# Performance work log

Hardware: AMD Instinct MI355X
Metric: run time of the kernel (lower is better)

Reference implementation:

```python
import jax, jax.numpy as jnp
import numpy as np

N_PARTS = 4
HIDDEN = 256
NUM_FREQS = 10
IN_DIM = 3
EMB_DIM = IN_DIM * (1 + 2 * NUM_FREQS)  # 63
PART_DIM = HIDDEN // N_PARTS


def _embed(x):
    freqs = 2.0 ** jnp.arange(NUM_FREQS, dtype=x.dtype)        # [F]
    xf = x[..., None, :] * freqs[:, None]                      # [..., F, 3]
    enc = jnp.stack([jnp.sin(xf), jnp.cos(xf)], axis=-2)       # [..., F, 2, 3]
    enc = enc.reshape(x.shape[:-1] + (NUM_FREQS * 2 * IN_DIM,))
    return jnp.concatenate([x, enc], axis=-1)                  # [..., 63]


def _masks():
    # contiguous 0/1 per-part neuron masks over the HIDDEN axis (ClassMaskCreator)
    m = np.zeros((N_PARTS, HIDDEN), dtype=np.float32)
    for p in range(N_PARTS):
        s = p * PART_DIM
        e = HIDDEN if p == N_PARTS - 1 else s + PART_DIM
        m[p, s:e] = 1.0
    return jnp.asarray(m)


def setup_inputs() -> dict:
    key = jax.random.key(0)
    ks = jax.random.split(key, 8)
    B, N = 1, 131072

    def lin(k, fan_in, fan_out):
        return jax.random.normal(k, (fan_in, fan_out), jnp.float32) / np.float32(np.sqrt(fan_in))

    return {
        "coords": jax.random.normal(ks[0], (B, N, IN_DIM), jnp.float32),
        "W0": lin(ks[1], EMB_DIM, HIDDEN), "b0": jnp.zeros((HIDDEN,), jnp.float32),
        "W1": lin(ks[2], HIDDEN, HIDDEN), "b1": jnp.zeros((HIDDEN,), jnp.float32),
        "W2": lin(ks[3], HIDDEN, HIDDEN), "b2": jnp.zeros((HIDDEN,), jnp.float32),
        "Wocc": lin(ks[4], HIDDEN, 1), "bocc": jnp.zeros((1,), jnp.float32),
        "Wc": jax.random.normal(ks[5], (N_PARTS, HIDDEN), jnp.float32) / np.float32(np.sqrt(HIDDEN)),
        "bc": jnp.zeros((N_PARTS,), jnp.float32),
    }


def reference(coords, W0, b0, W1, b1, W2, b2, Wocc, bocc, Wc, bc):
    masks = _masks()                                  # [P, H]
    x = _embed(coords) @ W0 + b0                      # [B, N, H]  (no activation after layer 0, per source)

    # occupancy trunk: relu(L1) -> relu(L2) -> occ head
    x_occ = jax.nn.relu(x @ W1 + b1)
    x_occ = jax.nn.relu(x_occ @ W2 + b2)
    occ = x_occ @ Wocc + bocc                         # [B, N, 1]

    # part branches. Loop iteration i=0 masks x; i=1 indexes temporal_part_output[1*part_id],
    # i.e. the i=0 outputs. The i=1 outputs (h2) are dead w.r.t. all returned values because
    # part_features[part_id] for part_id in 0..P-1 selects the first P (i=0) entries.
    h1 = [jax.nn.relu((x * masks[p]) @ W1 + b1) for p in range(N_PARTS)]  # [B, N, H] each

    # class heads: class_heads[p](h1[p] * mask_p).squeeze(0), concatenated on last dim
    cls = [jnp.squeeze((h1[p] * masks[p]) @ Wc[p][:, None] + bc[p], axis=0)
           for p in range(N_PARTS)]                   # [N, 1] each (B == 1)
    part_class = jnp.concatenate(cls, axis=-1)        # [N, P]

    return occ, part_class
```

## Files before the change

kernel.cpp:

```cpp
#include <hip/hip_runtime.h>


#define NPTS 131072
#define M_PB 128
#define AST 256

typedef _Float16 half8   __attribute__((ext_vector_type(8)));
typedef _Float16 half4_t __attribute__((ext_vector_type(4)));
typedef __fp16   fp16x2  __attribute__((ext_vector_type(2)));
typedef float    float4_t __attribute__((ext_vector_type(4)));

__global__ void prep(const float* __restrict__ W0, const float* __restrict__ W1,
                     const float* __restrict__ W2, _Float16* __restrict__ ws) {
  int id = blockIdx.x * 256 + threadIdx.x;
  _Float16 v;
  if (id < 16384) {
    int e = id, j = e & 7, l = (e >> 3) & 63, tn = (e >> 9) & 3, kb = (e >> 11) & 1, s = e >> 12;
    int k = kb * 32 + (l >> 4) * 8 + j, n = s * 64 + tn * 16 + (l & 15);
    v = (k < 63) ? (_Float16)W0[k * 256 + n] : (_Float16)0.f;
  } else if (id < 81920) {
    int e = id - 16384, j = e & 7, l = (e >> 3) & 63, tn = (e >> 9) & 3, kb = (e >> 11) & 7, s = e >> 14;
    int k = kb * 32 + (l >> 4) * 8 + j, n = s * 64 + tn * 16 + (l & 15);
    v = (_Float16)W1[k * 256 + n];
  } else {
    int e = id - 81920, j = e & 7, l = (e >> 3) & 63, tn = (e >> 9) & 3, kb = (e >> 11) & 7, s = e >> 14;
    int k = kb * 32 + (l >> 4) * 8 + j, n = s * 64 + tn * 16 + (l & 15);
    v = (_Float16)W2[k * 256 + n];
  }
  ws[id] = v;
}

__device__ __forceinline__ half4_t pack4(float a, float b, float cc, float d) {
  fp16x2 p0 = __builtin_amdgcn_cvt_pkrtz(a, b);
  fp16x2 p1 = __builtin_amdgcn_cvt_pkrtz(cc, d);
  half4_t h;
  h[0] = (_Float16)p0[0]; h[1] = (_Float16)p0[1];
  h[2] = (_Float16)p1[0]; h[3] = (_Float16)p1[1];
  return h;
}

__global__ __launch_bounds__(256, 2) void mlp_main(
    const float* __restrict__ coords,
    const _Float16* __restrict__ W0sw,
    const _Float16* __restrict__ W1sw,
    const _Float16* __restrict__ W2sw,
    const float* __restrict__ b0, const float* __restrict__ b1,
    const float* __restrict__ b2,
    const float* __restrict__ Wocc, const float* __restrict__ bocc,
    const float* __restrict__ Wc, const float* __restrict__ bc,
    float* __restrict__ out) {
  __shared__ _Float16 actX[M_PB * AST];
  __shared__ float occ_s[4][M_PB];

  const int t = threadIdx.x;
  const int w = t >> 6;
  const int l = t & 63;
  const int c = l & 15;
  const int q = l >> 4;
  const int sx = c & 7;
  const int m0 = blockIdx.x * M_PB;

  half8 a0[4], a1[4];
  {
    const _Float16* wb = W0sw + (size_t)w * 4096 + l * 8;
#pragma unroll
    for (int tn = 0; tn < 4; ++tn) {
      a0[tn] = *(const half8*)(wb + tn * 512);
      a1[tn] = *(const half8*)(wb + 2048 + tn * 512);
    }
  }

  {
    int m = t & 127, kh = (t >> 7) * 32;
    const int cb = (t >> 7) * 4;
    const int sm = m & 7;
    const float* cp = coords + (size_t)(m0 + m) * 3;
    float x0 = cp[0], x1 = cp[1], x2 = cp[2];
#pragma unroll
    for (int i = 0; i < 4; ++i) {
      float v[8];
#pragma unroll
      for (int u = 0; u < 8; ++u) {
        int k = kh + i * 8 + u;
        float r;
        if (k >= 63) r = 0.f;
        else if (k < 3) r = (k == 0) ? x0 : (k == 1 ? x1 : x2);
        else {
          int kk = k - 3;
          int f = kk / 6;
          int rem = kk - 6 * f;
          int s = (rem >= 3) ? 1 : 0;
          int i3 = rem - 3 * s;
          float xi = (i3 == 0) ? x0 : (i3 == 1 ? x1 : x2);
          float arg = xi * (float)(1 << f);
          float nn = rintf(arg * 0.15915494309189535f);
          float rr = fmaf(nn, -6.28318548202514648f, arg);
          rr = fmaf(nn, 1.7484555e-7f, rr);
          r = s ? __cosf(rr) : __sinf(rr);
        }
        v[u] = r;
      }
      half8 ev;
#pragma unroll
      for (int u = 0; u < 4; ++u) {
        fp16x2 p = __builtin_amdgcn_cvt_pkrtz(v[2 * u], v[2 * u + 1]);
        ev[2 * u] = (_Float16)p[0]; ev[2 * u + 1] = (_Float16)p[1];
      }
      *(half8*)&actX[m * AST + (((cb + i) ^ sm) << 3)] = ev;
    }
  }
  __syncthreads();

  float4_t acc[4][8];
  const _Float16* rp = actX + c * AST;

  {
#pragma unroll
    for (int tn = 0; tn < 4; ++tn) {
      float4_t bz = *(const float4_t*)(b0 + 64 * w + tn * 16 + q * 4);
#pragma unroll
      for (int tm = 0; tm < 8; ++tm) acc[tn][tm] = bz;
    }
#pragma unroll
    for (int kb = 0; kb < 2; ++kb) {
      const int cx = ((kb * 4 + q) ^ sx) << 3;
      half8 b[8];
#pragma unroll
      for (int tm = 0; tm < 8; ++tm) b[tm] = *(const half8*)(rp + tm * 16 * AST + cx);
#pragma unroll
      for (int tn = 0; tn < 4; ++tn)
#pragma unroll
        for (int tm = 0; tm < 8; ++tm)
          acc[tn][tm] = __builtin_amdgcn_mfma_f32_16x16x32_f16(
              kb ? a1[tn] : a0[tn], b[tm], acc[tn][tm], 0, 0, 0);
    }
  }
  __syncthreads();
#pragma unroll
  for (int tn = 0; tn < 4; ++tn) {
    const int sc = ((8 * w + 2 * tn + (q >> 1)) ^ sx) * 8 + (q & 1) * 4;
#pragma unroll
    for (int tm = 0; tm < 8; ++tm) {
      float4_t v = acc[tn][tm];
      *(half4_t*)&actX[(tm * 16 + c) * AST + sc] = pack4(v[0], v[1], v[2], v[3]);
    }
  }
  __syncthreads();

  {
    const _Float16* wb = W1sw + (size_t)w * 16384 + l * 8;
    const int w2 = 2 * w;
    float bcw = bc[w];
#pragma unroll
    for (int tn = 0; tn < 4; ++tn) {
      float4_t bz = *(const float4_t*)(b1 + 64 * w + tn * 16 + q * 4);
#pragma unroll
      for (int tm = 0; tm < 8; ++tm) acc[tn][tm] = bz;
    }
    auto kbof = [&](int j) {
      return (j < 2) ? (w2 + j) : ((j - 2) + ((j - 2) >= w2 ? 2 : 0));
    };
    half8 A[3][4];
#pragma unroll
    for (int p = 0; p < 3; ++p) {
      const _Float16* pa = wb + kbof(p) * 2048;
#pragma unroll
      for (int tn = 0; tn < 4; ++tn) A[p][tn] = *(const half8*)(pa + tn * 512);
    }
#pragma unroll
    for (int j = 0; j < 8; ++j) {
      const int kb = kbof(j);
      const int cx = ((kb * 4 + q) ^ sx) << 3;
      half8 b[8];
#pragma unroll
      for (int tm = 0; tm < 8; ++tm) b[tm] = *(const half8*)(rp + tm * 16 * AST + cx);
#pragma unroll
      for (int tn = 0; tn < 4; ++tn)
#pragma unroll
        for (int tm = 0; tm < 8; ++tm)
          acc[tn][tm] = __builtin_amdgcn_mfma_f32_16x16x32_f16(
              A[j % 3][tn], b[tm], acc[tn][tm], 0, 0, 0);
      if (j == 1) {
        float pcls[8] = {0.f, 0.f, 0.f, 0.f, 0.f, 0.f, 0.f, 0.f};
#pragma unroll
        for (int tn = 0; tn < 4; ++tn) {
          float4_t wcv = *(const float4_t*)(Wc + 256 * w + 64 * w + tn * 16 + q * 4);
#pragma unroll
          for (int tm = 0; tm < 8; ++tm) {
            float4_t v = acc[tn][tm];
#pragma unroll
            for (int r = 0; r < 4; ++r) pcls[tm] += fmaxf(v[r], 0.f) * wcv[r];
          }
        }
#pragma unroll
        for (int tm = 0; tm < 8; ++tm) {
          float s = pcls[tm];
          s += __shfl_xor(s, 16, 64);
          s += __shfl_xor(s, 32, 64);
          if (l < 16)
            out[(size_t)NPTS + (size_t)(m0 + tm * 16 + c) * 4 + w] = s + bcw;
        }
      }
      if (j + 3 < 8) {
        const _Float16* pa = wb + kbof(j + 3) * 2048;
#pragma unroll
        for (int tn = 0; tn < 4; ++tn) A[j % 3][tn] = *(const half8*)(pa + tn * 512);
      }
    }
  }
  __syncthreads();
#pragma unroll
  for (int tn = 0; tn < 4; ++tn) {
    const int sc = ((8 * w + 2 * tn + (q >> 1)) ^ sx) * 8 + (q & 1) * 4;
#pragma unroll
    for (int tm = 0; tm < 8; ++tm) {
      float4_t v = acc[tn][tm];
      *(half4_t*)&actX[(tm * 16 + c) * AST + sc] =
          pack4(fmaxf(v[0], 0.f), fmaxf(v[1], 0.f), fmaxf(v[2], 0.f), fmaxf(v[3], 0.f));
    }
  }
  __syncthreads();

  {
    const _Float16* wb = W2sw + (size_t)w * 16384 + l * 8;
#pragma unroll
    for (int tn = 0; tn < 4; ++tn) {
      float4_t bz = *(const float4_t*)(b2 + 64 * w + tn * 16 + q * 4);
#pragma unroll
      for (int tm = 0; tm < 8; ++tm) acc[tn][tm] = bz;
    }
    half8 A[3][4];
#pragma unroll
    for (int p = 0; p < 3; ++p)
#pragma unroll
      for (int tn = 0; tn < 4; ++tn)
        A[p][tn] = *(const half8*)(wb + p * 2048 + tn * 512);
#pragma unroll
    for (int kb = 0; kb < 8; ++kb) {
      const int cx = ((kb * 4 + q) ^ sx) << 3;
      half8 b[8];
#pragma unroll
      for (int tm = 0; tm < 8; ++tm) b[tm] = *(const half8*)(rp + tm * 16 * AST + cx);
#pragma unroll
      for (int tn = 0; tn < 4; ++tn)
#pragma unroll
        for (int tm = 0; tm < 8; ++tm)
          acc[tn][tm] = __builtin_amdgcn_mfma_f32_16x16x32_f16(
              A[kb % 3][tn], b[tm], acc[tn][tm], 0, 0, 0);
      if (kb + 3 < 8) {
#pragma unroll
        for (int tn = 0; tn < 4; ++tn)
          A[kb % 3][tn] = *(const half8*)(wb + (kb + 3) * 2048 + tn * 512);
      }
    }
    float pocc[8] = {0.f, 0.f, 0.f, 0.f, 0.f, 0.f, 0.f, 0.f};
#pragma unroll
    for (int tn = 0; tn < 4; ++tn) {
      float4_t wov = *(const float4_t*)(Wocc + 64 * w + tn * 16 + q * 4);
#pragma unroll
      for (int tm = 0; tm < 8; ++tm) {
        float4_t v = acc[tn][tm];
#pragma unroll
        for (int r = 0; r < 4; ++r) pocc[tm] += fmaxf(v[r], 0.f) * wov[r];
      }
    }
#pragma unroll
    for (int tm = 0; tm < 8; ++tm) {
      float s = pocc[tm];
      s += __shfl_xor(s, 16, 64);
      s += __shfl_xor(s, 32, 64);
      if (l < 16) occ_s[w][tm * 16 + c] = s;
    }
  }
  __syncthreads();
  if (t < M_PB) {
    out[m0 + t] = occ_s[0][t] + occ_s[1][t] + occ_s[2][t] + occ_s[3][t] + bocc[0];
  }
}

extern "C" void kernel_launch(void* const* d_in, const int* in_sizes, int n_in,
                              void* d_out, int out_size, void* d_ws, size_t ws_size,
                              hipStream_t stream) {
  const float* coords = (const float*)d_in[0];
  const float* W0   = (const float*)d_in[1];
  const float* b0   = (const float*)d_in[2];
  const float* W1   = (const float*)d_in[3];
  const float* b1   = (const float*)d_in[4];
  const float* W2   = (const float*)d_in[5];
  const float* b2   = (const float*)d_in[6];
  const float* Wocc = (const float*)d_in[7];
  const float* bocc = (const float*)d_in[8];
  const float* Wc   = (const float*)d_in[9];
  const float* bc   = (const float*)d_in[10];
  float* out = (float*)d_out;

  _Float16* ws = (_Float16*)d_ws;
  _Float16* W0sw = ws;
  _Float16* W1sw = ws + 16384;
  _Float16* W2sw = ws + 81920;

  prep<<<576, 256, 0, stream>>>(W0, W1, W2, ws);
  mlp_main<<<NPTS / M_PB, 256, 0, stream>>>(coords, W0sw, W1sw, W2sw,
                                            b0, b1, b2, Wocc, bocc, Wc, bc, out);
}
```

Baseline: 116.9 us.

## Ping-pong two warp groups across staggered MLP phases in 512-thread blocks

The kernel now launches 512-thread blocks, each holding two 256-thread groups with separate shared-memory activation buffers. Each block processes four 128-point tiles in a staggered schedule: one group runs the embedding and layer-0 phase while the other runs the layer-1 and layer-2 MFMA phases. The aim is to overlap the transcendental and VALU work with matrix-core work, and s_setprio is raised around the MFMA loops. In exchange, shared memory per block doubles, block-wide barriers now couple the two groups, and idle stagger steps are added at the start and end of the schedule.

```diff
diff --git a/kernel.cpp b/kernel.cpp
--- a/kernel.cpp
+++ b/kernel.cpp
@@ -39,7 +39,7 @@
   return h;
 }
 
-__global__ __launch_bounds__(256, 2) void mlp_main(
+__global__ __launch_bounds__(512, 2) void mlp_main(
     const float* __restrict__ coords,
     const _Float16* __restrict__ W0sw,
     const _Float16* __restrict__ W1sw,
@@ -49,232 +49,251 @@
     const float* __restrict__ Wocc, const float* __restrict__ bocc,
     const float* __restrict__ Wc, const float* __restrict__ bc,
     float* __restrict__ out) {
-  __shared__ _Float16 actX[M_PB * AST];
-  __shared__ float occ_s[4][M_PB];
+  __shared__ _Float16 actX[2][M_PB * AST];
+  __shared__ float occ_s[2][4][M_PB];
 
   const int t = threadIdx.x;
-  const int w = t >> 6;
+  const int g = t >> 8;
+  const int tl = t & 255;
+  const int w = (t >> 6) & 3;
   const int l = t & 63;
   const int c = l & 15;
   const int q = l >> 4;
   const int sx = c & 7;
-  const int m0 = blockIdx.x * M_PB;
-
+  const int blockBase = blockIdx.x * 512;
+
+  _Float16* aX = actX[g];
+  const _Float16* rp = aX + c * AST;
+
+  float4_t acc[4][8];
   half8 a0[4], a1[4];
-  {
-    const _Float16* wb = W0sw + (size_t)w * 4096 + l * 8;
-#pragma unroll
-    for (int tn = 0; tn < 4; ++tn) {
-      a0[tn] = *(const half8*)(wb + tn * 512);
-      a1[tn] = *(const half8*)(wb + 2048 + tn * 512);
+
+#pragma unroll 1
+  for (int i = 0; i < 5; ++i) {
+    const int step = i - g;
+    const bool isAct = (step >= 0) && (step < 4);
+    const bool isA = isAct && ((step & 1) == 0);
+    const bool isB = isAct && ((step & 1) == 1);
+    const int sp = isAct ? step : 0;
+    const int m0 = blockBase + 128 * (g + 2 * (sp >> 1));
+
+    if (isA) {
+      {
+        const _Float16* wb = W0sw + (size_t)w * 4096 + l * 8;
+#pragma unroll
+        for (int tn = 0; tn < 4; ++tn) {
+          a0[tn] = *(const half8*)(wb + tn * 512);
+          a1[tn] = *(const half8*)(wb + 2048 + tn * 512);
+        }
+      }
+      int m = tl & 127, kh = (tl >> 7) * 32;
+      const int cb = (tl >> 7) * 4;
+      const int sm = m & 7;
+      const float* cp = coords + (size_t)(m0 + m) * 3;
+      float x0 = cp[0], x1 = cp[1], x2 = cp[2];
+#pragma unroll
+      for (int ii = 0; ii < 4; ++ii) {
+        float v[8];
+#pragma unroll
+        for (int u = 0; u < 8; ++u) {
+          int k = kh + ii * 8 + u;
+          float r;
+          if (k >= 63) r = 0.f;
+          else if (k < 3) r = (k == 0) ? x0 : (k == 1 ? x1 : x2);
+          else {
+            int kk = k - 3;
+            int f = kk / 6;
+            int rem = kk - 6 * f;
+            int s = (rem >= 3) ? 1 : 0;
+            int i3 = rem - 3 * s;
+            float xi = (i3 == 0) ? x0 : (i3 == 1 ? x1 : x2);
+            float arg = xi * (float)(1 << f);
+            float nn = rintf(arg * 0.15915494309189535f);
+            float rr = fmaf(nn, -6.28318548202514648f, arg);
+            rr = fmaf(nn, 1.7484555e-7f, rr);
+            r = s ? __cosf(rr) : __sinf(rr);
+          }
+          v[u] = r;
+        }
+        half8 ev;
+#pragma unroll
+        for (int u = 0; u < 4; ++u) {
+          fp16x2 p = __builtin_amdgcn_cvt_pkrtz(v[2 * u], v[2 * u + 1]);
+          ev[2 * u] = (_Float16)p[0]; ev[2 * u + 1] = (_Float16)p[1];
+        }
+        *(half8*)&aX[m * AST + (((cb + ii) ^ sm) << 3)] = ev;
+      }
+    } else if (isB) {
+      const _Float16* wb = W1sw + (size_t)w * 16384 + l * 8;
+      const int w2 = 2 * w;
+      float bcw = bc[w];
+#pragma unroll
+      for (int tn = 0; tn < 4; ++tn) {
+        float4_t bz = *(const float4_t*)(b1 + 64 * w + tn * 16 + q * 4);
+#pragma unroll
+        for (int tm = 0; tm < 8; ++tm) acc[tn][tm] = bz;
+      }
+      auto kbof = [&](int j) {
+        return (j < 2) ? (w2 + j) : ((j - 2) + ((j - 2) >= w2 ? 2 : 0));
+      };
+      half8 A[3][4];
+#pragma unroll
+      for (int p = 0; p < 3; ++p) {
+        const _Float16* pa = wb + kbof(p) * 2048;
+#pragma unroll
+        for (int tn = 0; tn < 4; ++tn) A[p][tn] = *(const half8*)(pa + tn * 512);
+      }
+#pragma unroll
+      for (int j = 0; j < 8; ++j) {
+        const int kb = kbof(j);
+        const int cx = ((kb * 4 + q) ^ sx) << 3;
+        half8 b[8];
+#pragma unroll
+        for (int tm = 0; tm < 8; ++tm) b[tm] = *(const half8*)(rp + tm * 16 * AST + cx);
+        __builtin_amdgcn_s_setprio(1);
+#pragma unroll
+        for (int tn = 0; tn < 4; ++tn)
+#pragma unroll
+          for (int tm = 0; tm < 8; ++tm)
+            acc[tn][tm] = __builtin_amdgcn_mfma_f32_16x16x32_f16(
+                A[j % 3][tn], b[tm], acc[tn][tm], 0, 0, 0);
+        __builtin_amdgcn_s_setprio(0);
+        if (j == 1) {
+          float pcls[8] = {0.f, 0.f, 0.f, 0.f, 0.f, 0.f, 0.f, 0.f};
+#pragma unroll
+          for (int tn = 0; tn < 4; ++tn) {
+            float4_t wcv = *(const float4_t*)(Wc + 256 * w + 64 * w + tn * 16 + q * 4);
+#pragma unroll
+            for (int tm = 0; tm < 8; ++tm) {
+              float4_t v = acc[tn][tm];
+#pragma unroll
+              for (int r = 0; r < 4; ++r) pcls[tm] += fmaxf(v[r], 0.f) * wcv[r];
+            }
+          }
+#pragma unroll
+          for (int tm = 0; tm < 8; ++tm) {
+            float s = pcls[tm];
+            s += __shfl_xor(s, 16, 64);
+            s += __shfl_xor(s, 32, 64);
+            if (l < 16)
+              out[(size_t)NPTS + (size_t)(m0 + tm * 16 + c) * 4 + w] = s + bcw;
+          }
+        }
+        if (j + 3 < 8) {
+          const _Float16* pa = wb + kbof(j + 3) * 2048;
+#pragma unroll
+          for (int tn = 0; tn < 4; ++tn) A[j % 3][tn] = *(const half8*)(pa + tn * 512);
+        }
+      }
     }
-  }
-
-  {
-    int m = t & 127, kh = (t >> 7) * 32;
-    const int cb = (t >> 7) * 4;
-    const int sm = m & 7;
-    const float* cp = coords + (size_t)(m0 + m) * 3;
-    float x0 = cp[0], x1 = cp[1], x2 = cp[2];
-#pragma unroll
-    for (int i = 0; i < 4; ++i) {
-      float v[8];
-#pragma unroll
-      for (int u = 0; u < 8; ++u) {
-        int k = kh + i * 8 + u;
-        float r;
-        if (k >= 63) r = 0.f;
-        else if (k < 3) r = (k == 0) ? x0 : (k == 1 ? x1 : x2);
-        else {
-          int kk = k - 3;
-          int f = kk / 6;
-          int rem = kk - 6 * f;
-          int s = (rem >= 3) ? 1 : 0;
-          int i3 = rem - 3 * s;
-          float xi = (i3 == 0) ? x0 : (i3 == 1 ? x1 : x2);
-          float arg = xi * (float)(1 << f);
-          float nn = rintf(arg * 0.15915494309189535f);
-          float rr = fmaf(nn, -6.28318548202514648f, arg);
-          rr = fmaf(nn, 1.7484555e-7f, rr);
-          r = s ? __cosf(rr) : __sinf(rr);
-        }
-        v[u] = r;
-      }
-      half8 ev;
-#pragma unroll
-      for (int u = 0; u < 4; ++u) {
-        fp16x2 p = __builtin_amdgcn_cvt_pkrtz(v[2 * u], v[2 * u + 1]);
-        ev[2 * u] = (_Float16)p[0]; ev[2 * u + 1] = (_Float16)p[1];
-      }
-      *(half8*)&actX[m * AST + (((cb + i) ^ sm) << 3)] = ev;
+    __syncthreads();
+
+    if (isA) {
+#pragma unroll
+      for (int tn = 0; tn < 4; ++tn) {
+        float4_t bz = *(const float4_t*)(b0 + 64 * w + tn * 16 + q * 4);
+#pragma unroll
+        for (int tm = 0; tm < 8; ++tm) acc[tn][tm] = bz;
+      }
+#pragma unroll
+      for (int kb = 0; kb < 2; ++kb) {
+        const int cx = ((kb * 4 + q) ^ sx) << 3;
+        half8 b[8];
+#pragma unroll
+        for (int tm = 0; tm < 8; ++tm) b[tm] = *(const half8*)(rp + tm * 16 * AST + cx);
+#pragma unroll
+        for (int tn = 0; tn < 4; ++tn)
+#pragma unroll
+          for (int tm = 0; tm < 8; ++tm)
+            acc[tn][tm] = __builtin_amdgcn_mfma_f32_16x16x32_f16(
+                kb ? a1[tn] : a0[tn], b[tm], acc[tn][tm], 0, 0, 0);
+      }
+    } else if (isB) {
+#pragma unroll
+      for (int tn = 0; tn < 4; ++tn) {
+        const int sc = ((8 * w + 2 * tn + (q >> 1)) ^ sx) * 8 + (q & 1) * 4;
+#pragma unroll
+        for (int tm = 0; tm < 8; ++tm) {
+          float4_t v = acc[tn][tm];
+          *(half4_t*)&aX[(tm * 16 + c) * AST + sc] =
+              pack4(fmaxf(v[0], 0.f), fmaxf(v[1], 0.f), fmaxf(v[2], 0.f), fmaxf(v[3], 0.f));
+        }
+      }
     }
-  }
-  __syncthreads();
-
-  float4_t acc[4][8];
-  const _Float16* rp = actX + c * AST;
-
-  {
-#pragma unroll
-    for (int tn = 0; tn < 4; ++tn) {
-      float4_t bz = *(const float4_t*)(b0 + 64 * w + tn * 16 + q * 4);
-#pragma unroll
-      for (int tm = 0; tm < 8; ++tm) acc[tn][tm] = bz;
+    __syncthreads();
+
+    if (isA) {
+#pragma unroll
+      for (int tn = 0; tn < 4; ++tn) {
+        const int sc = ((8 * w + 2 * tn + (q >> 1)) ^ sx) * 8 + (q & 1) * 4;
+#pragma unroll
+        for (int tm = 0; tm < 8; ++tm) {
+          float4_t v = acc[tn][tm];
+          *(half4_t*)&aX[(tm * 16 + c) * AST + sc] = pack4(v[0], v[1], v[2], v[3]);
+        }
+      }
+    } else if (isB) {
+      const _Float16* wb = W2sw + (size_t)w * 16384 + l * 8;
+#pragma unroll
+      for (int tn = 0; tn < 4; ++tn) {
+        float4_t bz = *(const float4_t*)(b2 + 64 * w + tn * 16 + q * 4);
+#pragma unroll
+        for (int tm = 0; tm < 8; ++tm) acc[tn][tm] = bz;
+      }
+      half8 A[3][4];
+#pragma unroll
+      for (int p = 0; p < 3; ++p)
+#pragma unroll
+        for (int tn = 0; tn < 4; ++tn)
+          A[p][tn] = *(const half8*)(wb + p * 2048 + tn * 512);
+#pragma unroll
+      for (int kb = 0; kb < 8; ++kb) {
+        const int cx = ((kb * 4 + q) ^ sx) << 3;
+        half8 b[8];
+#pragma unroll
+        for (int tm = 0; tm < 8; ++tm) b[tm] = *(const half8*)(rp + tm * 16 * AST + cx);
+        __builtin_amdgcn_s_setprio(1);
+#pragma unroll
+        for (int tn = 0; tn < 4; ++tn)
+#pragma unroll
+          for (int tm = 0; tm < 8; ++tm)
+            acc[tn][tm] = __builtin_amdgcn_mfma_f32_16x16x32_f16(
+                A[kb % 3][tn], b[tm], acc[tn][tm], 0, 0, 0);
+        __builtin_amdgcn_s_setprio(0);
+        if (kb + 3 < 8) {
+#pragma unroll
+          for (int tn = 0; tn < 4; ++tn)
+            A[kb % 3][tn] = *(const half8*)(wb + (kb + 3) * 2048 + tn * 512);
+        }
+      }
+      float pocc[8] = {0.f, 0.f, 0.f, 0.f, 0.f, 0.f, 0.f, 0.f};
+#pragma unroll
+      for (int tn = 0; tn < 4; ++tn) {
+        float4_t wov = *(const float4_t*)(Wocc + 64 * w + tn * 16 + q * 4);
+#pragma unroll
+        for (int tm = 0; tm < 8; ++tm) {
+          float4_t v = acc[tn][tm];
+#pragma unroll
+          for (int r = 0; r < 4; ++r) pocc[tm] += fmaxf(v[r], 0.f) * wov[r];
+        }
+      }
+#pragma unroll
+      for (int tm = 0; tm < 8; ++tm) {
+        float s = pocc[tm];
+        s += __shfl_xor(s, 16, 64);
+        s += __shfl_xor(s, 32, 64);
+        if (l < 16) occ_s[g][w][tm * 16 + c] = s;
+      }
     }
-#pragma unroll
-    for (int kb = 0; kb < 2; ++kb) {
-      const int cx = ((kb * 4 + q) ^ sx) << 3;
-      half8 b[8];
-#pragma unroll
-      for (int tm = 0; tm < 8; ++tm) b[tm] = *(const half8*)(rp + tm * 16 * AST + cx);
-#pragma unroll
-      for (int tn = 0; tn < 4; ++tn)
-#pragma unroll
-        for (int tm = 0; tm < 8; ++tm)
-          acc[tn][tm] = __builtin_amdgcn_mfma_f32_16x16x32_f16(
-              kb ? a1[tn] : a0[tn], b[tm], acc[tn][tm], 0, 0, 0);
+    __syncthreads();
+
+    if (isB) {
+      if (tl < M_PB) {
+        out[m0 + tl] = occ_s[g][0][tl] + occ_s[g][1][tl] +
+                       occ_s[g][2][tl] + occ_s[g][3][tl] + bocc[0];
+      }
     }
-  }
-  __syncthreads();
-#pragma unroll
-  for (int tn = 0; tn < 4; ++tn) {
-    const int sc = ((8 * w + 2 * tn + (q >> 1)) ^ sx) * 8 + (q & 1) * 4;
-#pragma unroll
-    for (int tm = 0; tm < 8; ++tm) {
-      float4_t v = acc[tn][tm];
-      *(half4_t*)&actX[(tm * 16 + c) * AST + sc] = pack4(v[0], v[1], v[2], v[3]);
-    }
-  }
-  __syncthreads();
-
-  {
-    const _Float16* wb = W1sw + (size_t)w * 16384 + l * 8;
-    const int w2 = 2 * w;
-    float bcw = bc[w];
-#pragma unroll
-    for (int tn = 0; tn < 4; ++tn) {
-      float4_t bz = *(const float4_t*)(b1 + 64 * w + tn * 16 + q * 4);
-#pragma unroll
-      for (int tm = 0; tm < 8; ++tm) acc[tn][tm] = bz;
-    }
-    auto kbof = [&](int j) {
-      return (j < 2) ? (w2 + j) : ((j - 2) + ((j - 2) >= w2 ? 2 : 0));
-    };
-    half8 A[3][4];
-#pragma unroll
-    for (int p = 0; p < 3; ++p) {
-      const _Float16* pa = wb + kbof(p) * 2048;
-#pragma unroll
-      for (int tn = 0; tn < 4; ++tn) A[p][tn] = *(const half8*)(pa + tn * 512);
-    }
-#pragma unroll
-    for (int j = 0; j < 8; ++j) {
-      const int kb = kbof(j);
-      const int cx = ((kb * 4 + q) ^ sx) << 3;
-      half8 b[8];
-#pragma unroll
-      for (int tm = 0; tm < 8; ++tm) b[tm] = *(const half8*)(rp + tm * 16 * AST + cx);
-#pragma unroll
-      for (int tn = 0; tn < 4; ++tn)
-#pragma unroll
-        for (int tm = 0; tm < 8; ++tm)
-          acc[tn][tm] = __builtin_amdgcn_mfma_f32_16x16x32_f16(
-              A[j % 3][tn], b[tm], acc[tn][tm], 0, 0, 0);
-      if (j == 1) {
-        float pcls[8] = {0.f, 0.f, 0.f, 0.f, 0.f, 0.f, 0.f, 0.f};
-#pragma unroll
-        for (int tn = 0; tn < 4; ++tn) {
-          float4_t wcv = *(const float4_t*)(Wc + 256 * w + 64 * w + tn * 16 + q * 4);
-#pragma unroll
-          for (int tm = 0; tm < 8; ++tm) {
-            float4_t v = acc[tn][tm];
-#pragma unroll
-            for (int r = 0; r < 4; ++r) pcls[tm] += fmaxf(v[r], 0.f) * wcv[r];
-          }
-        }
-#pragma unroll
-        for (int tm = 0; tm < 8; ++tm) {
-          float s = pcls[tm];
-          s += __shfl_xor(s, 16, 64);
-          s += __shfl_xor(s, 32, 64);
-          if (l < 16)
-            out[(size_t)NPTS + (size_t)(m0 + tm * 16 + c) * 4 + w] = s + bcw;
-        }
-      }
-      if (j + 3 < 8) {
-        const _Float16* pa = wb + kbof(j + 3) * 2048;
-#pragma unroll
-        for (int tn = 0; tn < 4; ++tn) A[j % 3][tn] = *(const half8*)(pa + tn * 512);
-      }
-    }
-  }
-  __syncthreads();
-#pragma unroll
-  for (int tn = 0; tn < 4; ++tn) {
-    const int sc = ((8 * w + 2 * tn + (q >> 1)) ^ sx) * 8 + (q & 1) * 4;
-#pragma unroll
-    for (int tm = 0; tm < 8; ++tm) {
-      float4_t v = acc[tn][tm];
-      *(half4_t*)&actX[(tm * 16 + c) * AST + sc] =
-          pack4(fmaxf(v[0], 0.f), fmaxf(v[1], 0.f), fmaxf(v[2], 0.f), fmaxf(v[3], 0.f));
-    }
-  }
-  __syncthreads();
-
-  {
-    const _Float16* wb = W2sw + (size_t)w * 16384 + l * 8;
-#pragma unroll
-    for (int tn = 0; tn < 4; ++tn) {
-      float4_t bz = *(const float4_t*)(b2 + 64 * w + tn * 16 + q * 4);
-#pragma unroll
-      for (int tm = 0; tm < 8; ++tm) acc[tn][tm] = bz;
-    }
-    half8 A[3][4];
-#pragma unroll
-    for (int p = 0; p < 3; ++p)
-#pragma unroll
-      for (int tn = 0; tn < 4; ++tn)
-        A[p][tn] = *(const half8*)(wb + p * 2048 + tn * 512);
-#pragma unroll
-    for (int kb = 0; kb < 8; ++kb) {
-      const int cx = ((kb * 4 + q) ^ sx) << 3;
-      half8 b[8];
-#pragma unroll
-      for (int tm = 0; tm < 8; ++tm) b[tm] = *(const half8*)(rp + tm * 16 * AST + cx);
-#pragma unroll
-      for (int tn = 0; tn < 4; ++tn)
-#pragma unroll
-        for (int tm = 0; tm < 8; ++tm)
-          acc[tn][tm] = __builtin_amdgcn_mfma_f32_16x16x32_f16(
-              A[kb % 3][tn], b[tm], acc[tn][tm], 0, 0, 0);
-      if (kb + 3 < 8) {
-#pragma unroll
-        for (int tn = 0; tn < 4; ++tn)
-          A[kb % 3][tn] = *(const half8*)(wb + (kb + 3) * 2048 + tn * 512);
-      }
-    }
-    float pocc[8] = {0.f, 0.f, 0.f, 0.f, 0.f, 0.f, 0.f, 0.f};
-#pragma unroll
-    for (int tn = 0; tn < 4; ++tn) {
-      float4_t wov = *(const float4_t*)(Wocc + 64 * w + tn * 16 + q * 4);
-#pragma unroll
-      for (int tm = 0; tm < 8; ++tm) {
-        float4_t v = acc[tn][tm];
-#pragma unroll
-        for (int r = 0; r < 4; ++r) pocc[tm] += fmaxf(v[r], 0.f) * wov[r];
-      }
-    }
-#pragma unroll
-    for (int tm = 0; tm < 8; ++tm) {
-      float s = pocc[tm];
-      s += __shfl_xor(s, 16, 64);
-      s += __shfl_xor(s, 32, 64);
-      if (l < 16) occ_s[w][tm * 16 + c] = s;
-    }
-  }
-  __syncthreads();
-  if (t < M_PB) {
-    out[m0 + t] = occ_s[0][t] + occ_s[1][t] + occ_s[2][t] + occ_s[3][t] + bocc[0];
+    __syncthreads();
   }
 }
 
@@ -300,6 +319,6 @@
   _Float16* W2sw = ws + 81920;
 
   prep<<<576, 256, 0, stream>>>(W0, W1, W2, ws);
-  mlp_main<<<NPTS / M_PB, 256, 0, stream>>>(coords, W0sw, W1sw, W2sw,
-                                            b0, b1, b2, Wocc, bocc, Wc, bc, out);
+  mlp_main<<<NPTS / 512, 512, 0, stream>>>(coords, W0sw, W1sw, W2sw,
+                                           b0, b1, b2, Wocc, bocc, Wc, bc, out);
 }
```

Measured after the change: 221.1 us. 89.1% more time.

## Split positional encoding into a separate kernel and load MFMA operands directly

Applied to the files above, without the earlier changes.

Adds a standalone kernel that computes the fp16 positional encoding for all points into workspace. The main MLP kernel then loads the layer-0 B operands straight from global memory into registers, which removes the in-kernel sin/cos work and the LDS staging and sync before layer 0. The intent is to shorten the serial prologue of each block. The cost is an extra launch and a global round trip of about 16 MB of encoding, and the old path is kept as a fallback when the workspace is too small.

```diff
diff --git a/kernel.cpp b/kernel.cpp
--- a/kernel.cpp
+++ b/kernel.cpp
@@ -31,15 +31,260 @@
 }
 
 __device__ __forceinline__ half4_t pack4(float a, float b, float cc, float d) {
-  fp16x2 p0 = __builtin_amdgcn_cvt_pkrtz(a, b);
-  fp16x2 p1 = __builtin_amdgcn_cvt_pkrtz(cc, d);
-  half4_t h;
-  h[0] = (_Float16)p0[0]; h[1] = (_Float16)p0[1];
-  h[2] = (_Float16)p1[0]; h[3] = (_Float16)p1[1];
-  return h;
-}
-
-__global__ __launch_bounds__(256, 2) void mlp_main(
+  union { half4_t h; fp16x2 p[2]; } u;
+  u.p[0] = __builtin_amdgcn_cvt_pkrtz(a, b);
+  u.p[1] = __builtin_amdgcn_cvt_pkrtz(cc, d);
+  return u.h;
+}
+
+__device__ __forceinline__ float pe_val(int k, float x0, float x1, float x2) {
+  float r;
+  if (k >= 63) r = 0.f;
+  else if (k < 3) r = (k == 0) ? x0 : (k == 1 ? x1 : x2);
+  else {
+    int kk = k - 3;
+    int f = kk / 6;
+    int rem = kk - 6 * f;
+    int s = (rem >= 3) ? 1 : 0;
+    int i3 = rem - 3 * s;
+    float xi = (i3 == 0) ? x0 : (i3 == 1 ? x1 : x2);
+    float arg = xi * (float)(1 << f);
+    float nn = rintf(arg * 0.15915494309189535f);
+    float rr = fmaf(nn, -6.28318548202514648f, arg);
+    rr = fmaf(nn, 1.7484555e-7f, rr);
+    r = s ? __cosf(rr) : __sinf(rr);
+  }
+  return r;
+}
+
+__global__ __launch_bounds__(256) void pe(const float* __restrict__ coords,
+                                          _Float16* __restrict__ eg) {
+  int id = blockIdx.x * 256 + threadIdx.x;
+  int m = id >> 2, s = id & 3;
+  const float* cp = coords + (size_t)m * 3;
+  float x0 = cp[0], x1 = cp[1], x2 = cp[2];
+  int kh = s * 16;
+#pragma unroll
+  for (int i = 0; i < 2; ++i) {
+    float v[8];
+#pragma unroll
+    for (int u = 0; u < 8; ++u) v[u] = pe_val(kh + i * 8 + u, x0, x1, x2);
+    half8 ev;
+#pragma unroll
+    for (int u = 0; u < 4; ++u) {
+      fp16x2 p = __builtin_amdgcn_cvt_pkrtz(v[2 * u], v[2 * u + 1]);
+      ev[2 * u] = (_Float16)p[0]; ev[2 * u + 1] = (_Float16)p[1];
+    }
+    *(half8*)(eg + (size_t)m * 64 + kh + i * 8) = ev;
+  }
+}
+
+__global__ __launch_bounds__(256, 2) void mlp_main_g(
+    const _Float16* __restrict__ eg,
+    const _Float16* __restrict__ W0sw,
+    const _Float16* __restrict__ W1sw,
+    const _Float16* __restrict__ W2sw,
+    const float* __restrict__ b0, const float* __restrict__ b1,
+    const float* __restrict__ b2,
+    const float* __restrict__ Wocc, const float* __restrict__ bocc,
+    const float* __restrict__ Wc, const float* __restrict__ bc,
+    float* __restrict__ out) {
+  __shared__ _Float16 actX[M_PB * AST];
+  __shared__ float occ_s[4][M_PB];
+
+  const int t = threadIdx.x;
+  const int w = t >> 6;
+  const int l = t & 63;
+  const int c = l & 15;
+  const int q = l >> 4;
+  const int sx = c & 7;
+  const int m0 = blockIdx.x * M_PB;
+
+  half8 e0[8], e1[8];
+  {
+    const _Float16* ep = eg + (size_t)(m0 + c) * 64 + q * 8;
+#pragma unroll
+    for (int tm = 0; tm < 8; ++tm) {
+      e0[tm] = *(const half8*)(ep + tm * 1024);
+      e1[tm] = *(const half8*)(ep + tm * 1024 + 32);
+    }
+  }
+  half8 a0[4], a1[4];
+  {
+    const _Float16* wb = W0sw + (size_t)w * 4096 + l * 8;
+#pragma unroll
+    for (int tn = 0; tn < 4; ++tn) {
+      a0[tn] = *(const half8*)(wb + tn * 512);
+      a1[tn] = *(const half8*)(wb + 2048 + tn * 512);
+    }
+  }
+
+  float4_t acc[4][8];
+  const _Float16* rp = actX + c * AST;
+
+  {
+#pragma unroll
+    for (int tn = 0; tn < 4; ++tn) {
+      float4_t bz = *(const float4_t*)(b0 + 64 * w + tn * 16 + q * 4);
+#pragma unroll
+      for (int tm = 0; tm < 8; ++tm) acc[tn][tm] = bz;
+    }
+#pragma unroll
+    for (int tn = 0; tn < 4; ++tn)
+#pragma unroll
+      for (int tm = 0; tm < 8; ++tm)
+        acc[tn][tm] = __builtin_amdgcn_mfma_f32_16x16x32_f16(
+            a0[tn], e0[tm], acc[tn][tm], 0, 0, 0);
+#pragma unroll
+    for (int tn = 0; tn < 4; ++tn)
+#pragma unroll
+      for (int tm = 0; tm < 8; ++tm)
+        acc[tn][tm] = __builtin_amdgcn_mfma_f32_16x16x32_f16(
+            a1[tn], e1[tm], acc[tn][tm], 0, 0, 0);
+  }
+#pragma unroll
+  for (int tn = 0; tn < 4; ++tn) {
+    const int sc = ((8 * w + 2 * tn + (q >> 1)) ^ sx) * 8 + (q & 1) * 4;
+#pragma unroll
+    for (int tm = 0; tm < 8; ++tm) {
+      float4_t v = acc[tn][tm];
+      *(half4_t*)&actX[(tm * 16 + c) * AST + sc] = pack4(v[0], v[1], v[2], v[3]);
+    }
+  }
+  __syncthreads();
+
+  {
+    const _Float16* wb = W1sw + (size_t)w * 16384 + l * 8;
+    const int w2 = 2 * w;
+    float bcw = bc[w];
+#pragma unroll
+    for (int tn = 0; tn < 4; ++tn) {
+      float4_t bz = *(const float4_t*)(b1 + 64 * w + tn * 16 + q * 4);
+#pragma unroll
+      for (int tm = 0; tm < 8; ++tm) acc[tn][tm] = bz;
+    }
+    auto kbof = [&](int j) {
+      return (j < 2) ? (w2 + j) : ((j - 2) + ((j - 2) >= w2 ? 2 : 0));
+    };
+    half8 A[3][4];
+#pragma unroll
+    for (int p = 0; p < 3; ++p) {
+      const _Float16* pa = wb + kbof(p) * 2048;
+#pragma unroll
+      for (int tn = 0; tn < 4; ++tn) A[p][tn] = *(const half8*)(pa + tn * 512);
+    }
+#pragma unroll
+    for (int j = 0; j < 8; ++j) {
+      const int kb = kbof(j);
+      const int cx = ((kb * 4 + q) ^ sx) << 3;
+      half8 b[8];
+#pragma unroll
+      for (int tm = 0; tm < 8; ++tm) b[tm] = *(const half8*)(rp + tm * 16 * AST + cx);
+#pragma unroll
+      for (int tn = 0; tn < 4; ++tn)
+#pragma unroll
+        for (int tm = 0; tm < 8; ++tm)
+          acc[tn][tm] = __builtin_amdgcn_mfma_f32_16x16x32_f16(
+              A[j % 3][tn], b[tm], acc[tn][tm], 0, 0, 0);
+      if (j == 1) {
+        float pcls[8] = {0.f, 0.f, 0.f, 0.f, 0.f, 0.f, 0.f, 0.f};
+#pragma unroll
+        for (int tn = 0; tn < 4; ++tn) {
+          float4_t wcv = *(const float4_t*)(Wc + 256 * w + 64 * w + tn * 16 + q * 4);
+#pragma unroll
+          for (int tm = 0; tm < 8; ++tm) {
+            float4_t v = acc[tn][tm];
+#pragma unroll
+            for (int r = 0; r < 4; ++r) pcls[tm] += fmaxf(v[r], 0.f) * wcv[r];
+          }
+        }
+#pragma unroll
+        for (int tm = 0; tm < 8; ++tm) {
+          float s = pcls[tm];
+          s += __shfl_xor(s, 16, 64);
+          s += __shfl_xor(s, 32, 64);
+          if (l < 16)
+            out[(size_t)NPTS + (size_t)(m0 + tm * 16 + c) * 4 + w] = s + bcw;
+        }
+      }
+      if (j + 3 < 8) {
+        const _Float16* pa = wb + kbof(j + 3) * 2048;
+#pragma unroll
+        for (int tn = 0; tn < 4; ++tn) A[j % 3][tn] = *(const half8*)(pa + tn * 512);
+      }
+    }
+  }
+  __syncthreads();
+#pragma unroll
+  for (int tn = 0; tn < 4; ++tn) {
+    const int sc = ((8 * w + 2 * tn + (q >> 1)) ^ sx) * 8 + (q & 1) * 4;
+#pragma unroll
+    for (int tm = 0; tm < 8; ++tm) {
+      float4_t v = acc[tn][tm];
+      *(half4_t*)&actX[(tm * 16 + c) * AST + sc] =
+          pack4(fmaxf(v[0], 0.f), fmaxf(v[1], 0.f), fmaxf(v[2], 0.f), fmaxf(v[3], 0.f));
+    }
+  }
+  __syncthreads();
+
+  {
+    const _Float16* wb = W2sw + (size_t)w * 16384 + l * 8;
+#pragma unroll
+    for (int tn = 0; tn < 4; ++tn) {
+      float4_t bz = *(const float4_t*)(b2 + 64 * w + tn * 16 + q * 4);
+#pragma unroll
+      for (int tm = 0; tm < 8; ++tm) acc[tn][tm] = bz;
+    }
+    half8 A[3][4];
+#pragma unroll
+    for (int p = 0; p < 3; ++p)
+#pragma unroll
+      for (int tn = 0; tn < 4; ++tn)
+        A[p][tn] = *(const half8*)(wb + p * 2048 + tn * 512);
+#pragma unroll
+    for (int kb = 0; kb < 8; ++kb) {
+      const int cx = ((kb * 4 + q) ^ sx) << 3;
+      half8 b[8];
+#pragma unroll
+      for (int tm = 0; tm < 8; ++tm) b[tm] = *(const half8*)(rp + tm * 16 * AST + cx);
+#pragma unroll
+      for (int tn = 0; tn < 4; ++tn)
+#pragma unroll
+        for (int tm = 0; tm < 8; ++tm)
+          acc[tn][tm] = __builtin_amdgcn_mfma_f32_16x16x32_f16(
+              A[kb % 3][tn], b[tm], acc[tn][tm], 0, 0, 0);
+      if (kb + 3 < 8) {
+#pragma unroll
+        for (int tn = 0; tn < 4; ++tn)
+          A[kb % 3][tn] = *(const half8*)(wb + (kb + 3) * 2048 + tn * 512);
+      }
+    }
+    float pocc[8] = {0.f, 0.f, 0.f, 0.f, 0.f, 0.f, 0.f, 0.f};
+#pragma unroll
+    for (int tn = 0; tn < 4; ++tn) {
+      float4_t wov = *(const float4_t*)(Wocc + 64 * w + tn * 16 + q * 4);
+#pragma unroll
+      for (int tm = 0; tm < 8; ++tm) {
+        float4_t v = acc[tn][tm];
+#pragma unroll
+        for (int r = 0; r < 4; ++r) pocc[tm] += fmaxf(v[r], 0.f) * wov[r];
+      }
+    }
+#pragma unroll
+    for (int tm = 0; tm < 8; ++tm) {
+      float s = pocc[tm];
+      s += __shfl_xor(s, 16, 64);
+      s += __shfl_xor(s, 32, 64);
+      if (l < 16) occ_s[w][tm * 16 + c] = s;
+    }
+  }
+  __syncthreads();
+  if (t < M_PB) {
+    out[m0 + t] = occ_s[0][t] + occ_s[1][t] + occ_s[2][t] + occ_s[3][t] + bocc[0];
+  }
+}
+
+__global__ __launch_bounds__(256, 2) void mlp_main_l(
     const float* __restrict__ coords,
     const _Float16* __restrict__ W0sw,
     const _Float16* __restrict__ W1sw,
@@ -69,7 +314,6 @@
       a1[tn] = *(const half8*)(wb + 2048 + tn * 512);
     }
   }
-
   {
     int m = t & 127, kh = (t >> 7) * 32;
     const int cb = (t >> 7) * 4;
@@ -80,26 +324,7 @@
     for (int i = 0; i < 4; ++i) {
       float v[8];
 #pragma unroll
-      for (int u = 0; u < 8; ++u) {
-        int k = kh + i * 8 + u;
-        float r;
-        if (k >= 63) r = 0.f;
-        else if (k < 3) r = (k == 0) ? x0 : (k == 1 ? x1 : x2);
-        else {
-          int kk = k - 3;
-          int f = kk / 6;
-          int rem = kk - 6 * f;
-          int s = (rem >= 3) ? 1 : 0;
-          int i3 = rem - 3 * s;
-          float xi = (i3 == 0) ? x0 : (i3 == 1 ? x1 : x2);
-          float arg = xi * (float)(1 << f);
-          float nn = rintf(arg * 0.15915494309189535f);
-          float rr = fmaf(nn, -6.28318548202514648f, arg);
-          rr = fmaf(nn, 1.7484555e-7f, rr);
-          r = s ? __cosf(rr) : __sinf(rr);
-        }
-        v[u] = r;
-      }
+      for (int u = 0; u < 8; ++u) v[u] = pe_val(kh + i * 8 + u, x0, x1, x2);
       half8 ev;
 #pragma unroll
       for (int u = 0; u < 4; ++u) {
@@ -299,7 +524,18 @@
   _Float16* W1sw = ws + 16384;
   _Float16* W2sw = ws + 81920;
 
+  const size_t wbytes = 147456 * sizeof(_Float16);
+  const size_t ebytes = (size_t)NPTS * 64 * sizeof(_Float16);
+
   prep<<<576, 256, 0, stream>>>(W0, W1, W2, ws);
-  mlp_main<<<NPTS / M_PB, 256, 0, stream>>>(coords, W0sw, W1sw, W2sw,
-                                            b0, b1, b2, Wocc, bocc, Wc, bc, out);
-}
+
+  if (ws_size >= wbytes + ebytes) {
+    _Float16* eg = (_Float16*)((char*)d_ws + wbytes);
+    pe<<<(NPTS * 4) / 256, 256, 0, stream>>>(coords, eg);
+    mlp_main_g<<<NPTS / M_PB, 256, 0, stream>>>(eg, W0sw, W1sw, W2sw,
+                                                b0, b1, b2, Wocc, bocc, Wc, bc, out);
+  } else {
+    mlp_main_l<<<NPTS / M_PB, 256, 0, stream>>>(coords, W0sw, W1sw, W2sw,
+                                                b0, b1, b2, Wocc, bocc, Wc, bc, out);
+  }
+}
```

Result: slower. 125.2 us (+7.1%).
